# Kernel tuning notes

Hardware: AMD Instinct MI355X
Metric: run time of the kernel (lower is better)

The kernel has to match this reference:

```python
import jax, jax.numpy as jnp
import numpy as np

K, D = 8192, 64
BETA, DECAY, EPS = 0.25, 0.99, 1e-05


def setup_inputs() -> dict:
    key = jax.random.key(0)
    k1, k2 = jax.random.split(key)
    z = jax.random.normal(k1, (8, 2048, D), dtype=jnp.float32)
    codebook = jax.random.normal(k2, (K, D), dtype=jnp.float32)
    ema_cluster_size = jnp.zeros((K,), dtype=jnp.float32)
    ema_weight_sum = codebook  # initialised as a clone of the codebook
    return {"z": z, "codebook": codebook,
            "ema_cluster_size": ema_cluster_size,
            "ema_weight_sum": ema_weight_sum}


def reference(z, codebook, ema_cluster_size, ema_weight_sum):
    B, Q, Dd = z.shape
    flat = z.reshape(-1, Dd)                      # [N, D]
    dist = (jnp.sum(flat * flat, axis=1, keepdims=True)
            - 2.0 * flat @ codebook.T
            + jnp.sum(codebook * codebook, axis=1))
    idx = jnp.argmin(dist, axis=1)                # [N]
    z_q = codebook[idx].reshape(B, Q, Dd)         # gather

    commit = jnp.mean((z - jax.lax.stop_gradient(z_q)) ** 2)
    codebk = jnp.mean((z_q - jax.lax.stop_gradient(z)) ** 2)
    vq_loss = BETA * commit + codebk

    # straight-through estimator
    z_q_st = z + jax.lax.stop_gradient(z_q - z)

    # EMA update (training path; pure scatter-add via segment_sum, no one-hot)
    cluster_size = jax.ops.segment_sum(jnp.ones_like(idx, dtype=flat.dtype), idx,
                                       num_segments=K)            # [K]
    dw = jax.ops.segment_sum(flat, idx, num_segments=K)           # [K, D]
    new_cs = ema_cluster_size * DECAY + cluster_size * (1.0 - DECAY)
    new_ws = ema_weight_sum * DECAY + dw * (1.0 - DECAY)
    n = jnp.sum(new_cs)
    smoothed = (new_cs + EPS) / (n + K * EPS) * n
    new_codebook = new_ws / smoothed[:, None]

    return (z_q_st, vq_loss, idx.reshape(B, Q), new_codebook, new_cs, new_ws)
```

## Files before the change

### kernel.cpp

```cpp
#include <hip/hip_runtime.h>
#include <hip/hip_bf16.h>


#define NQ 16384
#define KC 8192
#define DD 64
#define NSPLIT 8
#define CSPLIT (KC / NSPLIT)
#define GROUP 128
#define NGROUP (CSPLIT / GROUP)
#define NTILE (GROUP / 16)
#define IMGH 16384

#define SC_BLOCKS 256
#define SC_CODES (KC / SC_BLOCKS)

typedef _Float16 half8 __attribute__((ext_vector_type(8)));
typedef _Float16 half4v __attribute__((ext_vector_type(4)));
typedef float f32x4 __attribute__((ext_vector_type(4)));
typedef unsigned int u32;

__device__ __forceinline__ void async_copy16(const _Float16* g, _Float16* l) {
  __builtin_amdgcn_global_load_lds(
      (const __attribute__((address_space(1))) u32*)(const void*)g,
      (__attribute__((address_space(3))) u32*)(void*)l, 16, 0, 0);
}


__global__ __launch_bounds__(256) void k_prep(
    const float* __restrict__ cb, const float* __restrict__ ema_cs,
    _Float16* __restrict__ Cxs, float* __restrict__ nhcn,
    float* __restrict__ epart) {
  const int t = threadIdx.x;
  const int gid = blockIdx.x * 256 + t;
  const int c = gid >> 4;
  const int j4 = gid & 15;

  const f32x4 v = ((const f32x4*)cb)[gid];
  half4v hh, ll;
  float s = 0.f;
#pragma unroll
  for (int e = 0; e < 4; ++e) {
    const float f = v[e];
    const _Float16 h = (_Float16)f;
    hh[e] = h;
    ll[e] = (_Float16)(f - (float)h);
    s = fmaf(f, f, s);
  }
  const int r = c & 127;
  const int tt = r >> 4;
  const int n = r & 15;
  const int q = (j4 >> 1) & 3;
  const int ihalf = j4 & 1;
  const int frh = j4 >> 3;
  const int fs = frh * 4 + q;
  const int nw = n ^ fs;
  _Float16* img = Cxs + (size_t)(c >> 7) * IMGH;
  *(half4v*)(img + ((size_t)((tt * 4 + frh) * 64 + q * 16 + nw)) * 8 +
             ihalf * 4) = hh;
  *(half4v*)(img + ((size_t)((tt * 4 + frh + 2) * 64 + q * 16 + nw)) * 8 +
             ihalf * 4) = ll;

#pragma unroll
  for (int off = 1; off < 16; off <<= 1) s += __shfl_xor(s, off, 64);
  if (j4 == 0) nhcn[c] = -0.5f * s;

  if (blockIdx.x < 32) {
    float su = ema_cs[blockIdx.x * 256 + t];
#pragma unroll
    for (int off = 1; off < 64; off <<= 1) su += __shfl_xor(su, off, 64);
    __shared__ float ss[4];
    if ((t & 63) == 0) ss[t >> 6] = su;
    __syncthreads();
    if (t == 0) epart[blockIdx.x] = ss[0] + ss[1] + ss[2] + ss[3];
  }
}

__global__ __launch_bounds__(256, 4) void k_mfma(
    const float* __restrict__ z, const _Float16* __restrict__ Cxs,
    const float* __restrict__ nhcn, float* __restrict__ pmax,
    int* __restrict__ pidx) {
  __shared__ _Float16 Bs[IMGH];
  const int t = threadIdx.x;
  const int lane = t & 63;
  const int w = t >> 6;
  const int split = blockIdx.y;
  const int Qw = blockIdx.x * 128 + w * 32;
  const int n16 = lane & 15;
  const int quad = lane >> 4;

  const f32x4* __restrict__ z4 = (const f32x4*)z;
  half8 aH0[2], aH1[2], aL0[2], aL1[2];
#pragma unroll
  for (int qt = 0; qt < 2; ++qt) {
    const size_t row16 = (size_t)(Qw + qt * 16 + n16) * 16;
#pragma unroll
    for (int hf = 0; hf < 2; ++hf) {
      const size_t rb = row16 + hf * 8 + quad * 2;
      const f32x4 va = z4[rb];
      const f32x4 vb = z4[rb + 1];
      half8 H, L;
#pragma unroll
      for (int e = 0; e < 4; ++e) {
        const float fa = va[e], fb = vb[e];
        const _Float16 ha = (_Float16)fa, hb = (_Float16)fb;
        H[e] = ha; H[e + 4] = hb;
        L[e] = (_Float16)(fa - (float)ha);
        L[e + 4] = (_Float16)(fb - (float)hb);
      }
      if (hf == 0) { aH0[qt] = H; aL0[qt] = L; }
      else         { aH1[qt] = H; aL1[qt] = L; }
    }
  }

  float best[2][4];
  int bidx[2][4];
#pragma unroll
  for (int qt = 0; qt < 2; ++qt)
#pragma unroll
    for (int r = 0; r < 4; ++r) {
      best[qt][r] = -3.4e38f;
      bidx[qt][r] = 0;
    }

  const half8* __restrict__ Bs8 = (const half8*)Bs;

  for (int g = 0; g < NGROUP; ++g) {
    const int C0 = split * CSPLIT + g * GROUP;
    const _Float16* gimg = Cxs + (size_t)(split * NGROUP + g) * IMGH;
    __syncthreads();
#pragma unroll
    for (int p = 0; p < 8; ++p) {
      const int off = (t + 256 * p) * 8;
      async_copy16(gimg + off, Bs + off);
    }
    __syncthreads();
#pragma unroll
    for (int tt = 0; tt < NTILE; ++tt) {
      const int base = tt * 4 * 64 + quad * 16;
      const half8 b0 = Bs8[base + (n16 ^ quad)];
      const half8 b1 = Bs8[base + 64 + (n16 ^ (4 + quad))];
      const half8 b2 = Bs8[base + 128 + (n16 ^ quad)];
      const half8 b3 = Bs8[base + 192 + (n16 ^ (4 + quad))];
      const int c = C0 + tt * 16 + n16;
      const float nc = nhcn[c];
#pragma unroll
      for (int qt = 0; qt < 2; ++qt) {
        f32x4 acc = {nc, nc, nc, nc};
        acc = __builtin_amdgcn_mfma_f32_16x16x32_f16(aH0[qt], b0, acc, 0, 0, 0);
        acc = __builtin_amdgcn_mfma_f32_16x16x32_f16(aH1[qt], b1, acc, 0, 0, 0);
        acc = __builtin_amdgcn_mfma_f32_16x16x32_f16(aH0[qt], b2, acc, 0, 0, 0);
        acc = __builtin_amdgcn_mfma_f32_16x16x32_f16(aH1[qt], b3, acc, 0, 0, 0);
        acc = __builtin_amdgcn_mfma_f32_16x16x32_f16(aL0[qt], b0, acc, 0, 0, 0);
        acc = __builtin_amdgcn_mfma_f32_16x16x32_f16(aL1[qt], b1, acc, 0, 0, 0);
#pragma unroll
        for (int r = 0; r < 4; ++r) {
          const float u = acc[r];
          if (u > best[qt][r]) { best[qt][r] = u; bidx[qt][r] = c; }
        }
      }
    }
  }
#pragma unroll
  for (int qt = 0; qt < 2; ++qt)
#pragma unroll
    for (int r = 0; r < 4; ++r) {
      float u = best[qt][r];
      int c = bidx[qt][r];
#pragma unroll
      for (int off = 1; off < 16; off <<= 1) {
        const float u2 = __shfl_xor(u, off, 64);
        const int c2 = __shfl_xor(c, off, 64);
        if (u2 > u || (u2 == u && c2 < c)) { u = u2; c = c2; }
      }
      if (n16 == 0) {
        const int q = Qw + qt * 16 + quad * 4 + r;
        pmax[(size_t)split * NQ + q] = u;
        pidx[(size_t)split * NQ + q] = c;
      }
    }
}

__global__ __launch_bounds__(256) void k_assign(
    const float* __restrict__ z, const float* __restrict__ cb,
    const float* __restrict__ pmax, const int* __restrict__ pidx,
    float* __restrict__ out_zq, float* __restrict__ out_idx,
    int* __restrict__ idx_i, float* __restrict__ parts) {
  const int t = threadIdx.x;
  const int d = t & 63;
  const int w = t >> 6;
  const int q = blockIdx.x * 4 + w;

  const int s = d & 7;
  float v = pmax[(size_t)s * NQ + q];
  int i = pidx[(size_t)s * NQ + q];
#pragma unroll
  for (int off = 1; off < 8; off <<= 1) {
    const float v2 = __shfl_xor(v, off, 64);
    const int i2 = __shfl_xor(i, off, 64);
    if (v2 > v || (v2 == v && i2 < i)) { v = v2; i = i2; }
  }
  const int k = i;

  const float zv = z[(size_t)q * DD + d];
  const float cv = cb[(size_t)k * DD + d];
  out_zq[(size_t)q * DD + d] = cv;
  const float diff = zv - cv;
  float sq = diff * diff;
#pragma unroll
  for (int off = 1; off < 64; off <<= 1) sq += __shfl_xor(sq, off, 64);
  __shared__ float ss[4];
  if (d == 0) {
    out_idx[q] = (float)k;
    idx_i[q] = k;
    ss[w] = sq;
  }
  __syncthreads();
  if (t == 0) parts[blockIdx.x] = ss[0] + ss[1] + ss[2] + ss[3];
}

__global__ __launch_bounds__(256) void k_tail(
    const float* __restrict__ z, const int* __restrict__ idx_i,
    const float* __restrict__ ema_cs, const float* __restrict__ ema_ws,
    const float* __restrict__ epart, const float* __restrict__ parts,
    float* __restrict__ out_ncs, float* __restrict__ out_ncb,
    float* __restrict__ out_nws, float* __restrict__ out_loss) {
  __shared__ float acc[SC_CODES * 64];
  __shared__ int cnt[SC_CODES];
  const int t = threadIdx.x;
  const int k0 = blockIdx.x * SC_CODES;
  for (int i = t; i < SC_CODES * 64; i += 256) acc[i] = 0.f;
  if (t < SC_CODES) cnt[t] = 0;
  __syncthreads();

  const int w = t >> 6, lane = t & 63;
  const int qbase = w * (NQ / 4);
#pragma unroll 4
  for (int it = 0; it < NQ / 4 / 64; ++it) {
    const int q = qbase + it * 64 + lane;
    const int kv = idx_i[q];
    const bool hit = (unsigned)(kv - k0) < (unsigned)SC_CODES;
    unsigned long long m = __ballot(hit);
    while (m) {
      const int j = __ffsll(m) - 1;
      m &= m - 1;
      const int kj = __shfl(kv, j, 64);
      const int qj = qbase + it * 64 + j;
      const float zvj = z[(size_t)qj * DD + lane];
      atomicAdd(&acc[(kj - k0) * 64 + lane], zvj);
      if (lane == 0) atomicAdd(&cnt[kj - k0], 1);
    }
  }
  __syncthreads();

  float esum = 0.f;
#pragma unroll
  for (int b = 0; b < 32; ++b) esum += epart[b];
  const float n = 0.99f * esum + 0.01f * 16384.0f;

  for (int i = t; i < SC_CODES * 64; i += 256) {
    const int kl = i >> 6;
    const int k = k0 + kl;
    const float v = 0.99f * ema_cs[k] + 0.01f * (float)cnt[kl];
    const float smoothed = (v + 1e-5f) / (n + (float)KC * 1e-5f) * n;
    const float nws = 0.99f * ema_ws[(size_t)k * DD + (i & 63)] + 0.01f * acc[i];
    out_nws[(size_t)k0 * DD + i] = nws;
    out_ncb[(size_t)k0 * DD + i] = nws / smoothed;
  }
  if (t < SC_CODES)
    out_ncs[k0 + t] = 0.99f * ema_cs[k0 + t] + 0.01f * (float)cnt[t];

  if (blockIdx.x == 0) {
    __syncthreads();
    float s = 0.f;
    for (int i = t; i < 4096; i += 256) s += parts[i];
#pragma unroll
    for (int off = 1; off < 64; off <<= 1) s += __shfl_xor(s, off, 64);
    if ((t & 63) == 0) acc[t >> 6] = s;
    __syncthreads();
    if (t == 0)
      *out_loss = 1.25f * (acc[0] + acc[1] + acc[2] + acc[3]) *
                  (1.0f / 1048576.0f);
  }
}

extern "C" void kernel_launch(void* const* d_in, const int* in_sizes, int n_in,
                              void* d_out, int out_size, void* d_ws,
                              size_t ws_size, hipStream_t stream) {
  const float* z = (const float*)d_in[0];
  const float* cb = (const float*)d_in[1];
  const float* ema_cs = (const float*)d_in[2];
  const float* ema_ws = (const float*)d_in[3];

  float* out = (float*)d_out;
  float* zq_out = out;
  float* loss_out = out + 1048576;
  float* idx_out = out + 1048577;
  float* ncb_out = out + 1064961;
  float* ncs_out = out + 1589249;
  float* nws_out = out + 1597441;

  float* ws = (float*)d_ws;
  float* nhcn = ws;
  float* epart = ws + 8192;
  float* parts = ws + 8256;
  float* pmax = ws + 12352;
  int* pidx = (int*)(ws + 143424);
  int* idx_i = (int*)(ws + 274496);
  _Float16* Cxs = (_Float16*)(ws + 290880);

  k_prep<<<KC * 16 / 256, 256, 0, stream>>>(cb, ema_cs, Cxs, nhcn, epart);
  k_mfma<<<dim3(NQ / 128, NSPLIT), 256, 0, stream>>>(z, Cxs, nhcn, pmax, pidx);
  k_assign<<<NQ / 4, 256, 0, stream>>>(z, cb, pmax, pidx, zq_out, idx_out,
                                       idx_i, parts);
  k_tail<<<SC_BLOCKS, 256, 0, stream>>>(z, idx_i, ema_cs, ema_ws, epart, parts,
                                        ncs_out, ncb_out, nws_out, loss_out);
}
```

Baseline: 152.0 us.

## Fuse VQ pipeline into one persistent cooperative kernel with grid syncs

Merges the prep, distance/argmin MFMA, assign and EMA-tail kernels into one cooperative persistent kernel. Blocks loop over job indices and separate the stages with grid.sync(), which removes three kernel launches and the gaps between them. The tail stage now splits the codebook into 1024 jobs of 8 codes, so the idx array is rescanned more times in total. The MFMA stage runs with launch bounds allowing 2 blocks per CU instead of 4, so it may take several rounds and lose latency hiding. If the cooperative launch fails, the code falls back to the original four-kernel sequence.

Result: slower. 357.1 us (+134.9%).

```diff
diff --git a/kernel.cpp b/kernel.cpp
--- a/kernel.cpp
+++ b/kernel.cpp
@@ -1,5 +1,8 @@
 #include <hip/hip_runtime.h>
 #include <hip/hip_bf16.h>
+#include <hip/hip_cooperative_groups.h>
+
+namespace cg = cooperative_groups;
 
 
 #define NQ 16384
@@ -11,9 +14,12 @@
 #define NGROUP (CSPLIT / GROUP)
 #define NTILE (GROUP / 16)
 #define IMGH 16384
+#define MJOBS 1024
 
 #define SC_BLOCKS 256
 #define SC_CODES (KC / SC_BLOCKS)
+#define TJOBS 1024
+#define TC_CODES (KC / TJOBS)
 
 typedef _Float16 half8 __attribute__((ext_vector_type(8)));
 typedef _Float16 half4v __attribute__((ext_vector_type(4)));
@@ -27,15 +33,14 @@
 }
 
 
-__global__ __launch_bounds__(256) void k_prep(
-    const float* __restrict__ cb, const float* __restrict__ ema_cs,
-    _Float16* __restrict__ Cxs, float* __restrict__ nhcn,
-    float* __restrict__ epart) {
-  const int t = threadIdx.x;
-  const int gid = blockIdx.x * 256 + t;
+
+__device__ __forceinline__ void prep_job(int job, int t,
+                                         const float* __restrict__ cb,
+                                         _Float16* __restrict__ Cxs,
+                                         float* __restrict__ nhcn) {
+  const int gid = job * 256 + t;
   const int c = gid >> 4;
   const int j4 = gid & 15;
-
   const f32x4 v = ((const f32x4*)cb)[gid];
   half4v hh, ll;
   float s = 0.f;
@@ -60,34 +65,22 @@
              ihalf * 4) = hh;
   *(half4v*)(img + ((size_t)((tt * 4 + frh + 2) * 64 + q * 16 + nw)) * 8 +
              ihalf * 4) = ll;
-
 #pragma unroll
   for (int off = 1; off < 16; off <<= 1) s += __shfl_xor(s, off, 64);
   if (j4 == 0) nhcn[c] = -0.5f * s;
-
-  if (blockIdx.x < 32) {
-    float su = ema_cs[blockIdx.x * 256 + t];
-#pragma unroll
-    for (int off = 1; off < 64; off <<= 1) su += __shfl_xor(su, off, 64);
-    __shared__ float ss[4];
-    if ((t & 63) == 0) ss[t >> 6] = su;
-    __syncthreads();
-    if (t == 0) epart[blockIdx.x] = ss[0] + ss[1] + ss[2] + ss[3];
-  }
-}
-
-__global__ __launch_bounds__(256, 4) void k_mfma(
-    const float* __restrict__ z, const _Float16* __restrict__ Cxs,
-    const float* __restrict__ nhcn, float* __restrict__ pmax,
-    int* __restrict__ pidx) {
-  __shared__ _Float16 Bs[IMGH];
-  const int t = threadIdx.x;
+}
+
+__device__ __forceinline__ void mfma_job(
+    int job, int t, _Float16* Bs, const float* __restrict__ z,
+    const _Float16* __restrict__ Cxs, const float* __restrict__ nhcn,
+    float* __restrict__ pmax, int* __restrict__ pidx) {
   const int lane = t & 63;
   const int w = t >> 6;
-  const int split = blockIdx.y;
-  const int Qw = blockIdx.x * 128 + w * 32;
+  const int split = job & 7;
+  const int Qw = (job >> 3) * 128 + w * 32;
   const int n16 = lane & 15;
   const int quad = lane >> 4;
+  const half8* Bs8 = (const half8*)Bs;
 
   const f32x4* __restrict__ z4 = (const f32x4*)z;
   half8 aH0[2], aH1[2], aL0[2], aL1[2];
@@ -122,8 +115,6 @@
       best[qt][r] = -3.4e38f;
       bidx[qt][r] = 0;
     }
-
-  const half8* __restrict__ Bs8 = (const half8*)Bs;
 
   for (int g = 0; g < NGROUP; ++g) {
     const int C0 = split * CSPLIT + g * GROUP;
@@ -181,40 +172,190 @@
     }
 }
 
+__device__ __forceinline__ float assign_q(
+    int q, int d, const float* __restrict__ z, const float* __restrict__ cb,
+    const float* __restrict__ pmax, const int* __restrict__ pidx,
+    float* __restrict__ out_zq, float* __restrict__ out_idx,
+    int* __restrict__ idx_i) {
+  const int s = d & 7;
+  float v = pmax[(size_t)s * NQ + q];
+  int i = pidx[(size_t)s * NQ + q];
+#pragma unroll
+  for (int off = 1; off < 8; off <<= 1) {
+    const float v2 = __shfl_xor(v, off, 64);
+    const int i2 = __shfl_xor(i, off, 64);
+    if (v2 > v || (v2 == v && i2 < i)) { v = v2; i = i2; }
+  }
+  const int k = i;
+  const float zv = z[(size_t)q * DD + d];
+  const float cv = cb[(size_t)k * DD + d];
+  out_zq[(size_t)q * DD + d] = cv;
+  const float diff = zv - cv;
+  float sq = diff * diff;
+#pragma unroll
+  for (int off = 1; off < 64; off <<= 1) sq += __shfl_xor(sq, off, 64);
+  if (d == 0) {
+    out_idx[q] = (float)k;
+    idx_i[q] = k;
+  }
+  return sq;
+}
+
+template <int NCODES>
+__device__ __forceinline__ void tail_job(
+    int k0, int t, float* acc, int* cnt, const float* __restrict__ z,
+    const int* __restrict__ idx_i, const float* __restrict__ ema_cs,
+    const float* __restrict__ ema_ws, float n, float* __restrict__ out_ncs,
+    float* __restrict__ out_ncb, float* __restrict__ out_nws) {
+  const int w = t >> 6, lane = t & 63;
+  for (int i = t; i < NCODES * 64; i += 256) acc[i] = 0.f;
+  if (t < NCODES) cnt[t] = 0;
+  __syncthreads();
+  const int qbase = w * (NQ / 4);
+#pragma unroll 4
+  for (int it = 0; it < NQ / 4 / 64; ++it) {
+    const int q = qbase + it * 64 + lane;
+    const int kv = idx_i[q];
+    const bool hit = (unsigned)(kv - k0) < (unsigned)NCODES;
+    unsigned long long m = __ballot(hit);
+    while (m) {
+      const int j = __ffsll(m) - 1;
+      m &= m - 1;
+      const int kj = __shfl(kv, j, 64);
+      const int qj = qbase + it * 64 + j;
+      const float zvj = z[(size_t)qj * DD + lane];
+      atomicAdd(&acc[(kj - k0) * 64 + lane], zvj);
+      if (lane == 0) atomicAdd(&cnt[kj - k0], 1);
+    }
+  }
+  __syncthreads();
+  for (int i = t; i < NCODES * 64; i += 256) {
+    const int kl = i >> 6;
+    const int k = k0 + kl;
+    const float v = 0.99f * ema_cs[k] + 0.01f * (float)cnt[kl];
+    const float smoothed = (v + 1e-5f) / (n + (float)KC * 1e-5f) * n;
+    const float nws =
+        0.99f * ema_ws[(size_t)k * DD + (i & 63)] + 0.01f * acc[i];
+    out_nws[(size_t)k0 * DD + i] = nws;
+    out_ncb[(size_t)k0 * DD + i] = nws / smoothed;
+  }
+  if (t < NCODES)
+    out_ncs[k0 + t] = 0.99f * ema_cs[k0 + t] + 0.01f * (float)cnt[t];
+}
+
+
+__global__ __launch_bounds__(256, 2) void k_fused(
+    const float* __restrict__ z, const float* __restrict__ cb,
+    const float* __restrict__ ema_cs, const float* __restrict__ ema_ws,
+    float* __restrict__ zq_out, float* __restrict__ loss_out,
+    float* __restrict__ idx_out, float* __restrict__ ncb_out,
+    float* __restrict__ ncs_out, float* __restrict__ nws_out,
+    _Float16* __restrict__ Cxs, float* __restrict__ nhcn,
+    float* __restrict__ epart, float* __restrict__ parts,
+    float* __restrict__ pmax, int* __restrict__ pidx,
+    int* __restrict__ idx_i) {
+  cg::grid_group grid = cg::this_grid();
+  __shared__ __align__(16) char ldsraw[32768];
+  const int b = blockIdx.x;
+  const int G = gridDim.x;
+  const int t = threadIdx.x;
+  const int w = t >> 6;
+  const int lane = t & 63;
+
+  for (int job = b; job < 512; job += G) {
+    prep_job(job, t, cb, Cxs, nhcn);
+    if (job < 32) {
+      float su = ema_cs[job * 256 + t];
+#pragma unroll
+      for (int off = 1; off < 64; off <<= 1) su += __shfl_xor(su, off, 64);
+      float* ss = (float*)ldsraw;
+      __syncthreads();
+      if (lane == 0) ss[w] = su;
+      __syncthreads();
+      if (t == 0) epart[job] = ss[0] + ss[1] + ss[2] + ss[3];
+    }
+  }
+  grid.sync();
+
+  for (int job = b; job < MJOBS; job += G)
+    mfma_job(job, t, (_Float16*)ldsraw, z, Cxs, nhcn, pmax, pidx);
+  grid.sync();
+
+  for (int job = b; job < 1024; job += G) {
+    float sqacc = 0.f;
+#pragma unroll
+    for (int j = 0; j < 4; ++j)
+      sqacc += assign_q(job * 16 + w * 4 + j, lane, z, cb, pmax, pidx, zq_out,
+                        idx_out, idx_i);
+    float* ss = (float*)ldsraw;
+    __syncthreads();
+    if (lane == 0) ss[w] = sqacc;
+    __syncthreads();
+    if (t == 0) parts[job] = ss[0] + ss[1] + ss[2] + ss[3];
+  }
+  grid.sync();
+
+  float esum = 0.f;
+#pragma unroll
+  for (int e = 0; e < 32; ++e) esum += epart[e];
+  const float n = 0.99f * esum + 0.01f * 16384.0f;
+  float* acc = (float*)ldsraw;
+  int* cnt = (int*)(ldsraw + TC_CODES * 64 * 4);
+  for (int job = b; job < TJOBS; job += G) {
+    __syncthreads();
+    tail_job<TC_CODES>(job * TC_CODES, t, acc, cnt, z, idx_i, ema_cs, ema_ws,
+                       n, ncs_out, ncb_out, nws_out);
+  }
+  if (b == 0) {
+    __syncthreads();
+    float s = 0.f;
+    for (int i = t; i < 1024; i += 256) s += parts[i];
+#pragma unroll
+    for (int off = 1; off < 64; off <<= 1) s += __shfl_xor(s, off, 64);
+    if (lane == 0) acc[w] = s;
+    __syncthreads();
+    if (t == 0)
+      *loss_out = 1.25f * (acc[0] + acc[1] + acc[2] + acc[3]) *
+                  (1.0f / 1048576.0f);
+  }
+}
+
+
+__global__ __launch_bounds__(256) void k_prep(
+    const float* __restrict__ cb, const float* __restrict__ ema_cs,
+    _Float16* __restrict__ Cxs, float* __restrict__ nhcn,
+    float* __restrict__ epart) {
+  const int t = threadIdx.x;
+  prep_job(blockIdx.x, t, cb, Cxs, nhcn);
+  if (blockIdx.x < 32) {
+    float su = ema_cs[blockIdx.x * 256 + t];
+#pragma unroll
+    for (int off = 1; off < 64; off <<= 1) su += __shfl_xor(su, off, 64);
+    __shared__ float ss[4];
+    if ((t & 63) == 0) ss[t >> 6] = su;
+    __syncthreads();
+    if (t == 0) epart[blockIdx.x] = ss[0] + ss[1] + ss[2] + ss[3];
+  }
+}
+
+__global__ __launch_bounds__(256, 4) void k_mfma(
+    const float* __restrict__ z, const _Float16* __restrict__ Cxs,
+    const float* __restrict__ nhcn, float* __restrict__ pmax,
+    int* __restrict__ pidx) {
+  __shared__ __align__(16) _Float16 Bs[IMGH];
+  mfma_job(blockIdx.x, threadIdx.x, Bs, z, Cxs, nhcn, pmax, pidx);
+}
+
 __global__ __launch_bounds__(256) void k_assign(
     const float* __restrict__ z, const float* __restrict__ cb,
     const float* __restrict__ pmax, const int* __restrict__ pidx,
     float* __restrict__ out_zq, float* __restrict__ out_idx,
     int* __restrict__ idx_i, float* __restrict__ parts) {
   const int t = threadIdx.x;
-  const int d = t & 63;
-  const int w = t >> 6;
-  const int q = blockIdx.x * 4 + w;
-
-  const int s = d & 7;
-  float v = pmax[(size_t)s * NQ + q];
-  int i = pidx[(size_t)s * NQ + q];
-#pragma unroll
-  for (int off = 1; off < 8; off <<= 1) {
-    const float v2 = __shfl_xor(v, off, 64);
-    const int i2 = __shfl_xor(i, off, 64);
-    if (v2 > v || (v2 == v && i2 < i)) { v = v2; i = i2; }
-  }
-  const int k = i;
-
-  const float zv = z[(size_t)q * DD + d];
-  const float cv = cb[(size_t)k * DD + d];
-  out_zq[(size_t)q * DD + d] = cv;
-  const float diff = zv - cv;
-  float sq = diff * diff;
-#pragma unroll
-  for (int off = 1; off < 64; off <<= 1) sq += __shfl_xor(sq, off, 64);
+  const float sq = assign_q(blockIdx.x * 4 + (t >> 6), t & 63, z, cb, pmax,
+                            pidx, out_zq, out_idx, idx_i);
   __shared__ float ss[4];
-  if (d == 0) {
-    out_idx[q] = (float)k;
-    idx_i[q] = k;
-    ss[w] = sq;
-  }
+  if ((t & 63) == 0) ss[t >> 6] = sq;
   __syncthreads();
   if (t == 0) parts[blockIdx.x] = ss[0] + ss[1] + ss[2] + ss[3];
 }
@@ -228,48 +369,12 @@
   __shared__ float acc[SC_CODES * 64];
   __shared__ int cnt[SC_CODES];
   const int t = threadIdx.x;
-  const int k0 = blockIdx.x * SC_CODES;
-  for (int i = t; i < SC_CODES * 64; i += 256) acc[i] = 0.f;
-  if (t < SC_CODES) cnt[t] = 0;
-  __syncthreads();
-
-  const int w = t >> 6, lane = t & 63;
-  const int qbase = w * (NQ / 4);
-#pragma unroll 4
-  for (int it = 0; it < NQ / 4 / 64; ++it) {
-    const int q = qbase + it * 64 + lane;
-    const int kv = idx_i[q];
-    const bool hit = (unsigned)(kv - k0) < (unsigned)SC_CODES;
-    unsigned long long m = __ballot(hit);
-    while (m) {
-      const int j = __ffsll(m) - 1;
-      m &= m - 1;
-      const int kj = __shfl(kv, j, 64);
-      const int qj = qbase + it * 64 + j;
-      const float zvj = z[(size_t)qj * DD + lane];
-      atomicAdd(&acc[(kj - k0) * 64 + lane], zvj);
-      if (lane == 0) atomicAdd(&cnt[kj - k0], 1);
-    }
-  }
-  __syncthreads();
-
   float esum = 0.f;
 #pragma unroll
-  for (int b = 0; b < 32; ++b) esum += epart[b];
+  for (int e = 0; e < 32; ++e) esum += epart[e];
   const float n = 0.99f * esum + 0.01f * 16384.0f;
-
-  for (int i = t; i < SC_CODES * 64; i += 256) {
-    const int kl = i >> 6;
-    const int k = k0 + kl;
-    const float v = 0.99f * ema_cs[k] + 0.01f * (float)cnt[kl];
-    const float smoothed = (v + 1e-5f) / (n + (float)KC * 1e-5f) * n;
-    const float nws = 0.99f * ema_ws[(size_t)k * DD + (i & 63)] + 0.01f * acc[i];
-    out_nws[(size_t)k0 * DD + i] = nws;
-    out_ncb[(size_t)k0 * DD + i] = nws / smoothed;
-  }
-  if (t < SC_CODES)
-    out_ncs[k0 + t] = 0.99f * ema_cs[k0 + t] + 0.01f * (float)cnt[t];
-
+  tail_job<SC_CODES>(blockIdx.x * SC_CODES, t, acc, cnt, z, idx_i, ema_cs,
+                     ema_ws, n, out_ncs, out_ncb, out_nws);
   if (blockIdx.x == 0) {
     __syncthreads();
     float s = 0.f;
@@ -309,10 +414,28 @@
   int* idx_i = (int*)(ws + 274496);
   _Float16* Cxs = (_Float16*)(ws + 290880);
 
-  k_prep<<<KC * 16 / 256, 256, 0, stream>>>(cb, ema_cs, Cxs, nhcn, epart);
-  k_mfma<<<dim3(NQ / 128, NSPLIT), 256, 0, stream>>>(z, Cxs, nhcn, pmax, pidx);
-  k_assign<<<NQ / 4, 256, 0, stream>>>(z, cb, pmax, pidx, zq_out, idx_out,
-                                       idx_i, parts);
-  k_tail<<<SC_BLOCKS, 256, 0, stream>>>(z, idx_i, ema_cs, ema_ws, epart, parts,
-                                        ncs_out, ncb_out, nws_out, loss_out);
-}
+  int occ = 0;
+  hipError_t oe = hipOccupancyMaxActiveBlocksPerMultiprocessor(
+      &occ, (const void*)k_fused, 256, 0);
+  int G = (oe == hipSuccess) ? occ * 256 : 0;
+  if (G > 1024) G = 1024;
+  bool coop_done = false;
+  if (G >= 8) {
+    void* args[] = {&z,       &cb,      &ema_cs,  &ema_ws, &zq_out, &loss_out,
+                    &idx_out, &ncb_out, &ncs_out, &nws_out, &Cxs,   &nhcn,
+                    &epart,   &parts,   &pmax,    &pidx,    &idx_i};
+    hipError_t le = hipLaunchCooperativeKernel((const void*)k_fused, dim3(G),
+                                               dim3(256), args, 0, stream);
+    coop_done = (le == hipSuccess);
+  }
+
+  if (!coop_done) {
+    k_prep<<<KC * 16 / 256, 256, 0, stream>>>(cb, ema_cs, Cxs, nhcn, epart);
+    k_mfma<<<dim3(MJOBS), 256, 0, stream>>>(z, Cxs, nhcn, pmax, pidx);
+    k_assign<<<NQ / 4, 256, 0, stream>>>(z, cb, pmax, pidx, zq_out, idx_out,
+                                         idx_i, parts);
+    k_tail<<<SC_BLOCKS, 256, 0, stream>>>(z, idx_i, ema_cs, ema_ws, epart,
+                                          parts, ncs_out, ncb_out, nws_out,
+                                          loss_out);
+  }
+}
```

## Merge split-argmin via packed 64-bit atomicMax and fuse assign with EMA tail

Applied to the files above, without the earlier changes.

The distance kernel now writes each query's best (score, index) as one order-preserving 64-bit key into a per-query slot with atomicMax. This replaces the per-split partial arrays and the separate cross-split reduction. The old assign and EMA-tail kernels become one launch whose blocks split into two roles: gather/loss blocks, and per-code scatter-accumulate blocks that decode the index from the low word. The grid is also flattened so that the eight splits of a query tile launch next to each other. This removes one kernel launch and intermediate traffic, at the cost of global atomics on the query keys and the loss scalar, which both have to be zeroed in the prep kernel.

Result: no change. 152.1 us (+0.1%).

```diff
diff --git a/kernel.cpp b/kernel.cpp
--- a/kernel.cpp
+++ b/kernel.cpp
@@ -11,14 +11,17 @@
 #define NGROUP (CSPLIT / GROUP)
 #define NTILE (GROUP / 16)
 #define IMGH 16384
-
-#define SC_BLOCKS 256
-#define SC_CODES (KC / SC_BLOCKS)
+#define MJOBS 1024
+
+#define AQ_BLOCKS 256
+#define TL_BLOCKS 256
+#define TL_CODES (KC / TL_BLOCKS)
 
 typedef _Float16 half8 __attribute__((ext_vector_type(8)));
 typedef _Float16 half4v __attribute__((ext_vector_type(4)));
 typedef float f32x4 __attribute__((ext_vector_type(4)));
 typedef unsigned int u32;
+typedef unsigned long long u64;
 
 __device__ __forceinline__ void async_copy16(const _Float16* g, _Float16* l) {
   __builtin_amdgcn_global_load_lds(
@@ -26,13 +29,21 @@
       (__attribute__((address_space(3))) u32*)(void*)l, 16, 0, 0);
 }
 
+__device__ __forceinline__ u64 pack_uc(float u, int c) {
+  u32 ub = __float_as_uint(u);
+  ub = (ub & 0x80000000u) ? ~ub : (ub | 0x80000000u);
+  return ((u64)ub << 32) | (u64)(0xFFFFFFFFu - (u32)c);
+}
+
 
 __global__ __launch_bounds__(256) void k_prep(
     const float* __restrict__ cb, const float* __restrict__ ema_cs,
     _Float16* __restrict__ Cxs, float* __restrict__ nhcn,
-    float* __restrict__ epart) {
+    float* __restrict__ epart, u64* __restrict__ qmax,
+    float* __restrict__ loss_out) {
+  const int b = blockIdx.x;
   const int t = threadIdx.x;
-  const int gid = blockIdx.x * 256 + t;
+  const int gid = b * 256 + t;
   const int c = gid >> 4;
   const int j4 = gid & 15;
 
@@ -60,34 +71,36 @@
              ihalf * 4) = hh;
   *(half4v*)(img + ((size_t)((tt * 4 + frh + 2) * 64 + q * 16 + nw)) * 8 +
              ihalf * 4) = ll;
-
 #pragma unroll
   for (int off = 1; off < 16; off <<= 1) s += __shfl_xor(s, off, 64);
   if (j4 == 0) nhcn[c] = -0.5f * s;
 
-  if (blockIdx.x < 32) {
-    float su = ema_cs[blockIdx.x * 256 + t];
+  if (t < 32) qmax[b * 32 + t] = 0ull;
+  if (b == 0 && t == 0) *loss_out = 0.f;
+
+  if (b < 32) {
+    float su = ema_cs[b * 256 + t];
 #pragma unroll
     for (int off = 1; off < 64; off <<= 1) su += __shfl_xor(su, off, 64);
     __shared__ float ss[4];
     if ((t & 63) == 0) ss[t >> 6] = su;
     __syncthreads();
-    if (t == 0) epart[blockIdx.x] = ss[0] + ss[1] + ss[2] + ss[3];
+    if (t == 0) epart[b] = ss[0] + ss[1] + ss[2] + ss[3];
   }
 }
 
 __global__ __launch_bounds__(256, 4) void k_mfma(
     const float* __restrict__ z, const _Float16* __restrict__ Cxs,
-    const float* __restrict__ nhcn, float* __restrict__ pmax,
-    int* __restrict__ pidx) {
-  __shared__ _Float16 Bs[IMGH];
+    const float* __restrict__ nhcn, u64* __restrict__ qmax) {
+  __shared__ __align__(16) _Float16 Bs[IMGH];
   const int t = threadIdx.x;
   const int lane = t & 63;
   const int w = t >> 6;
-  const int split = blockIdx.y;
-  const int Qw = blockIdx.x * 128 + w * 32;
+  const int split = blockIdx.x & 7;
+  const int Qw = (blockIdx.x >> 3) * 128 + w * 32;
   const int n16 = lane & 15;
   const int quad = lane >> 4;
+  const half8* Bs8 = (const half8*)Bs;
 
   const f32x4* __restrict__ z4 = (const f32x4*)z;
   half8 aH0[2], aH1[2], aL0[2], aL1[2];
@@ -122,8 +135,6 @@
       best[qt][r] = -3.4e38f;
       bidx[qt][r] = 0;
     }
-
-  const half8* __restrict__ Bs8 = (const half8*)Bs;
 
   for (int g = 0; g < NGROUP; ++g) {
     const int C0 = split * CSPLIT + g * GROUP;
@@ -175,112 +186,89 @@
       }
       if (n16 == 0) {
         const int q = Qw + qt * 16 + quad * 4 + r;
-        pmax[(size_t)split * NQ + q] = u;
-        pidx[(size_t)split * NQ + q] = c;
-      }
-    }
-}
-
-__global__ __launch_bounds__(256) void k_assign(
+        atomicMax(&qmax[q], pack_uc(u, c));
+      }
+    }
+}
+
+__global__ __launch_bounds__(256) void k_post(
     const float* __restrict__ z, const float* __restrict__ cb,
-    const float* __restrict__ pmax, const int* __restrict__ pidx,
-    float* __restrict__ out_zq, float* __restrict__ out_idx,
-    int* __restrict__ idx_i, float* __restrict__ parts) {
+    const float* __restrict__ ema_cs, const float* __restrict__ ema_ws,
+    const u32* __restrict__ qlow, const float* __restrict__ epart,
+    float* __restrict__ zq_out, float* __restrict__ idx_out,
+    float* __restrict__ ncb_out, float* __restrict__ ncs_out,
+    float* __restrict__ nws_out, float* __restrict__ loss_out) {
+  __shared__ float acc[TL_CODES * 64];
+  __shared__ int cnt[TL_CODES];
+  const int b = blockIdx.x;
   const int t = threadIdx.x;
-  const int d = t & 63;
   const int w = t >> 6;
-  const int q = blockIdx.x * 4 + w;
-
-  const int s = d & 7;
-  float v = pmax[(size_t)s * NQ + q];
-  int i = pidx[(size_t)s * NQ + q];
-#pragma unroll
-  for (int off = 1; off < 8; off <<= 1) {
-    const float v2 = __shfl_xor(v, off, 64);
-    const int i2 = __shfl_xor(i, off, 64);
-    if (v2 > v || (v2 == v && i2 < i)) { v = v2; i = i2; }
-  }
-  const int k = i;
-
-  const float zv = z[(size_t)q * DD + d];
-  const float cv = cb[(size_t)k * DD + d];
-  out_zq[(size_t)q * DD + d] = cv;
-  const float diff = zv - cv;
-  float sq = diff * diff;
-#pragma unroll
-  for (int off = 1; off < 64; off <<= 1) sq += __shfl_xor(sq, off, 64);
-  __shared__ float ss[4];
-  if (d == 0) {
-    out_idx[q] = (float)k;
-    idx_i[q] = k;
-    ss[w] = sq;
-  }
-  __syncthreads();
-  if (t == 0) parts[blockIdx.x] = ss[0] + ss[1] + ss[2] + ss[3];
-}
-
-__global__ __launch_bounds__(256) void k_tail(
-    const float* __restrict__ z, const int* __restrict__ idx_i,
-    const float* __restrict__ ema_cs, const float* __restrict__ ema_ws,
-    const float* __restrict__ epart, const float* __restrict__ parts,
-    float* __restrict__ out_ncs, float* __restrict__ out_ncb,
-    float* __restrict__ out_nws, float* __restrict__ out_loss) {
-  __shared__ float acc[SC_CODES * 64];
-  __shared__ int cnt[SC_CODES];
-  const int t = threadIdx.x;
-  const int k0 = blockIdx.x * SC_CODES;
-  for (int i = t; i < SC_CODES * 64; i += 256) acc[i] = 0.f;
-  if (t < SC_CODES) cnt[t] = 0;
-  __syncthreads();
-
-  const int w = t >> 6, lane = t & 63;
-  const int qbase = w * (NQ / 4);
+  const int lane = t & 63;
+
+  if (b < AQ_BLOCKS) {
+    float sqacc = 0.f;
+    const int qbase = b * 64 + w * 16;
 #pragma unroll 4
-  for (int it = 0; it < NQ / 4 / 64; ++it) {
-    const int q = qbase + it * 64 + lane;
-    const int kv = idx_i[q];
-    const bool hit = (unsigned)(kv - k0) < (unsigned)SC_CODES;
-    unsigned long long m = __ballot(hit);
-    while (m) {
-      const int j = __ffsll(m) - 1;
-      m &= m - 1;
-      const int kj = __shfl(kv, j, 64);
-      const int qj = qbase + it * 64 + j;
-      const float zvj = z[(size_t)qj * DD + lane];
-      atomicAdd(&acc[(kj - k0) * 64 + lane], zvj);
-      if (lane == 0) atomicAdd(&cnt[kj - k0], 1);
-    }
-  }
-  __syncthreads();
-
-  float esum = 0.f;
-#pragma unroll
-  for (int b = 0; b < 32; ++b) esum += epart[b];
-  const float n = 0.99f * esum + 0.01f * 16384.0f;
-
-  for (int i = t; i < SC_CODES * 64; i += 256) {
-    const int kl = i >> 6;
-    const int k = k0 + kl;
-    const float v = 0.99f * ema_cs[k] + 0.01f * (float)cnt[kl];
-    const float smoothed = (v + 1e-5f) / (n + (float)KC * 1e-5f) * n;
-    const float nws = 0.99f * ema_ws[(size_t)k * DD + (i & 63)] + 0.01f * acc[i];
-    out_nws[(size_t)k0 * DD + i] = nws;
-    out_ncb[(size_t)k0 * DD + i] = nws / smoothed;
-  }
-  if (t < SC_CODES)
-    out_ncs[k0 + t] = 0.99f * ema_cs[k0 + t] + 0.01f * (float)cnt[t];
-
-  if (blockIdx.x == 0) {
-    __syncthreads();
-    float s = 0.f;
-    for (int i = t; i < 4096; i += 256) s += parts[i];
-#pragma unroll
-    for (int off = 1; off < 64; off <<= 1) s += __shfl_xor(s, off, 64);
-    if ((t & 63) == 0) acc[t >> 6] = s;
+    for (int j = 0; j < 16; ++j) {
+      const int q = qbase + j;
+      const int k = (int)(0xFFFFFFFFu - qlow[2 * q]);
+      const float zv = z[(size_t)q * DD + lane];
+      const float cv = cb[(size_t)k * DD + lane];
+      zq_out[(size_t)q * DD + lane] = cv;
+      const float diff = zv - cv;
+      sqacc = fmaf(diff, diff, sqacc);
+      if (lane == 0) idx_out[q] = (float)k;
+    }
+#pragma unroll
+    for (int off = 1; off < 64; off <<= 1) sqacc += __shfl_xor(sqacc, off, 64);
+    if (lane == 0) acc[w] = sqacc;
     __syncthreads();
     if (t == 0)
-      *out_loss = 1.25f * (acc[0] + acc[1] + acc[2] + acc[3]) *
-                  (1.0f / 1048576.0f);
+      atomicAdd(loss_out,
+                1.25f * (acc[0] + acc[1] + acc[2] + acc[3]) *
+                    (1.0f / 1048576.0f));
+  } else {
+    const int k0 = (b - AQ_BLOCKS) * TL_CODES;
+    for (int i = t; i < TL_CODES * 64; i += 256) acc[i] = 0.f;
+    if (t < TL_CODES) cnt[t] = 0;
+    __syncthreads();
+
+    const int qbase = w * (NQ / 4);
+#pragma unroll 4
+    for (int it = 0; it < NQ / 4 / 64; ++it) {
+      const int q = qbase + it * 64 + lane;
+      const int kv = (int)(0xFFFFFFFFu - qlow[2 * q]);
+      const bool hit = (unsigned)(kv - k0) < (unsigned)TL_CODES;
+      unsigned long long m = __ballot(hit);
+      while (m) {
+        const int j = __ffsll(m) - 1;
+        m &= m - 1;
+        const int kj = __shfl(kv, j, 64);
+        const int qj = qbase + it * 64 + j;
+        const float zvj = z[(size_t)qj * DD + lane];
+        atomicAdd(&acc[(kj - k0) * 64 + lane], zvj);
+        if (lane == 0) atomicAdd(&cnt[kj - k0], 1);
+      }
+    }
+    __syncthreads();
+
+    float esum = 0.f;
+#pragma unroll
+    for (int e = 0; e < 32; ++e) esum += epart[e];
+    const float n = 0.99f * esum + 0.01f * 16384.0f;
+
+    for (int i = t; i < TL_CODES * 64; i += 256) {
+      const int kl = i >> 6;
+      const int k = k0 + kl;
+      const float v = 0.99f * ema_cs[k] + 0.01f * (float)cnt[kl];
+      const float smoothed = (v + 1e-5f) / (n + (float)KC * 1e-5f) * n;
+      const float nws =
+          0.99f * ema_ws[(size_t)k * DD + (i & 63)] + 0.01f * acc[i];
+      nws_out[(size_t)k0 * DD + i] = nws;
+      ncb_out[(size_t)k0 * DD + i] = nws / smoothed;
+    }
+    if (t < TL_CODES)
+      ncs_out[k0 + t] = 0.99f * ema_cs[k0 + t] + 0.01f * (float)cnt[t];
   }
 }
 
@@ -303,16 +291,13 @@
   float* ws = (float*)d_ws;
   float* nhcn = ws;
   float* epart = ws + 8192;
-  float* parts = ws + 8256;
-  float* pmax = ws + 12352;
-  int* pidx = (int*)(ws + 143424);
-  int* idx_i = (int*)(ws + 274496);
-  _Float16* Cxs = (_Float16*)(ws + 290880);
-
-  k_prep<<<KC * 16 / 256, 256, 0, stream>>>(cb, ema_cs, Cxs, nhcn, epart);
-  k_mfma<<<dim3(NQ / 128, NSPLIT), 256, 0, stream>>>(z, Cxs, nhcn, pmax, pidx);
-  k_assign<<<NQ / 4, 256, 0, stream>>>(z, cb, pmax, pidx, zq_out, idx_out,
-                                       idx_i, parts);
-  k_tail<<<SC_BLOCKS, 256, 0, stream>>>(z, idx_i, ema_cs, ema_ws, epart, parts,
-                                        ncs_out, ncb_out, nws_out, loss_out);
-}
+  u64* qmax = (u64*)(ws + 8224);
+  _Float16* Cxs = (_Float16*)(ws + 40992);
+
+  k_prep<<<KC * 16 / 256, 256, 0, stream>>>(cb, ema_cs, Cxs, nhcn, epart,
+                                            qmax, loss_out);
+  k_mfma<<<MJOBS, 256, 0, stream>>>(z, Cxs, nhcn, qmax);
+  k_post<<<AQ_BLOCKS + TL_BLOCKS, 256, 0, stream>>>(
+      z, cb, ema_cs, ema_ws, (const u32*)qmax, epart, zq_out, idx_out,
+      ncb_out, ncs_out, nws_out, loss_out);
+}
```
